# Kernel optimization log

Measured on AMD Instinct MI355X. Metric: run time of the kernel, lower is better.

Reference implementation:

```python
import jax, jax.numpy as jnp
import numpy as np

DETECTIONS_PER_IMG = 36
NMS_THRESH = 0.5
SCORE_THRESH = 0.2
MIN_SIZE = 0.01
NMS_TOPK = 2048  # fixed candidate budget for jit-compatible NMS
BBOX_XFORM_CLIP = float(np.log(1000.0 / 16.0))
WX, WY, WW, WH = 10.0, 10.0, 5.0, 5.0  # torchvision BoxCoder weights


def _decode(reg, props):
    # reg: [N, C*4], props: [N, 4] -> decoded boxes [N, C, 4] (torchvision BoxCoder.decode)
    widths = props[:, 2] - props[:, 0]
    heights = props[:, 3] - props[:, 1]
    ctr_x = props[:, 0] + 0.5 * widths
    ctr_y = props[:, 1] + 0.5 * heights
    reg = reg.reshape(reg.shape[0], -1, 4)
    dx = reg[..., 0] / WX
    dy = reg[..., 1] / WY
    dw = jnp.minimum(reg[..., 2] / WW, BBOX_XFORM_CLIP)
    dh = jnp.minimum(reg[..., 3] / WH, BBOX_XFORM_CLIP)
    pcx = dx * widths[:, None] + ctr_x[:, None]
    pcy = dy * heights[:, None] + ctr_y[:, None]
    pw = jnp.exp(dw) * widths[:, None]
    ph = jnp.exp(dh) * heights[:, None]
    return jnp.stack([pcx - 0.5 * pw, pcy - 0.5 * ph,
                      pcx + 0.5 * pw, pcy + 0.5 * ph], axis=-1)


def _pairwise_iou(boxes):
    # boxes: [K, 4] -> IoU [K, K]
    area = (boxes[:, 2] - boxes[:, 0]) * (boxes[:, 3] - boxes[:, 1])
    lt = jnp.maximum(boxes[:, None, :2], boxes[None, :, :2])
    rb = jnp.minimum(boxes[:, None, 2:], boxes[None, :, 2:])
    wh = jnp.clip(rb - lt, 0.0)
    inter = wh[..., 0] * wh[..., 1]
    union = area[:, None] + area[None, :] - inter
    return jnp.where(union > 0, inter / union, 0.0)


def _per_image(logits, reg, props, feats, img_hw):
    # logits [N, C], reg [N, C*4], props [N, 4], feats [N, D], img_hw [2] (h, w)
    N, C = logits.shape
    boxes = _decode(reg, props)[:, 1:, :].reshape(-1, 4)     # drop background, [N*(C-1), 4]
    scores = jax.nn.softmax(logits, axis=-1)[:, 1:].reshape(-1)
    h = img_hw[0].astype(boxes.dtype)
    w = img_hw[1].astype(boxes.dtype)
    x1 = jnp.clip(boxes[:, 0], 0.0, w)
    y1 = jnp.clip(boxes[:, 1], 0.0, h)
    x2 = jnp.clip(boxes[:, 2], 0.0, w)
    y2 = jnp.clip(boxes[:, 3], 0.0, h)
    boxes = jnp.stack([x1, y1, x2, y2], axis=-1)
    # score threshold + remove_small_boxes as a validity mask
    valid = (scores > SCORE_THRESH) & ((x2 - x1) >= MIN_SIZE) & ((y2 - y1) >= MIN_SIZE)
    masked = jnp.where(valid, scores, -jnp.inf)
    top_s, top_i = jax.lax.top_k(masked, NMS_TOPK)          # candidates in score order
    tboxes = boxes[top_i]
    tvalid = jnp.isfinite(top_s)
    iou = _pairwise_iou(tboxes)                              # [K, K]
    ar = jnp.arange(NMS_TOPK)

    def body(i, keep):
        sup = keep[i] & (iou[i] > NMS_THRESH) & (ar > i)
        return keep & ~sup

    keep = jax.lax.fori_loop(0, NMS_TOPK, body, tvalid)
    # first DETECTIONS_PER_IMG kept candidates, in score order (stable sort: kept first)
    order = jnp.argsort(jnp.where(keep, 0, 1), stable=True)[:DETECTIONS_PER_IMG]
    sel_keep = keep[order]
    prop_idx = top_i[order] // (C - 1)                       # candidate -> proposal row
    out = feats[prop_idx] * sel_keep[:, None].astype(feats.dtype)  # zero-pad missing slots
    return out


def setup_inputs() -> dict:
    key = jax.random.key(0)
    k0, k1, k2, k3, k4 = jax.random.split(key, 5)
    B, N, C, D = 8, 1000, 91, 1024
    class_logits = jax.random.normal(k0, (B, N, C), dtype=jnp.float32) * 3.0
    box_regression = jax.random.normal(k1, (B, N, C * 4), dtype=jnp.float32) * 0.5
    xy = jax.random.uniform(k2, (B, N, 2), minval=0.0, maxval=700.0)
    wh = jax.random.uniform(k3, (B, N, 2), minval=20.0, maxval=100.0)
    proposals = jnp.concatenate([xy, xy + wh], axis=-1).astype(jnp.float32)
    box_features = jax.random.normal(k4, (B, N, D), dtype=jnp.float32)
    image_shapes = jnp.full((B, 2), 800, dtype=jnp.int32)
    return {"class_logits": class_logits, "box_regression": box_regression,
            "proposals": proposals, "box_features": box_features,
            "image_shapes": image_shapes}


def reference(class_logits, box_regression, proposals, box_features, image_shapes):
    # returns [B, DETECTIONS_PER_IMG, D]
    return jax.vmap(_per_image)(class_logits, box_regression, proposals,
                                box_features, image_shapes)
```

## Files before the change

kernel.cpp:

```cpp
#include <hip/hip_runtime.h>
#include <stdint.h>

#define B 8
#define N 1000
#define C 91
#define NC 90
#define D 1024
#define KMAX 2048
#define PAD 4096
#define DETS 36
#define SCORE_THRESH 0.2f
#define NMS_THRESH 0.5f
#define MIN_SIZE 0.01f
#define XFORM_CLIP 4.135166556742356f

__device__ __forceinline__ void decode_clip(const float* __restrict__ rg,
                                            float wdt, float hgt, float cx, float cy,
                                            float W, float H,
                                            float& x1, float& y1, float& x2, float& y2) {
    float dx = rg[0] / 10.0f;
    float dy = rg[1] / 10.0f;
    float dw = fminf(rg[2] / 5.0f, XFORM_CLIP);
    float dh = fminf(rg[3] / 5.0f, XFORM_CLIP);
    float pcx = dx * wdt + cx;
    float pcy = dy * hgt + cy;
    float pw  = expf(dw) * wdt;
    float ph  = expf(dh) * hgt;
    x1 = fminf(fmaxf(pcx - 0.5f * pw, 0.0f), W);
    y1 = fminf(fmaxf(pcy - 0.5f * ph, 0.0f), H);
    x2 = fminf(fmaxf(pcx + 0.5f * pw, 0.0f), W);
    y2 = fminf(fmaxf(pcy + 0.5f * ph, 0.0f), H);
}

__global__ __launch_bounds__(256) void k_score(const float* __restrict__ logits,
                        const float* __restrict__ reg,
                        const float* __restrict__ props,
                        const int* __restrict__ img_hw,
                        unsigned long long* __restrict__ keys) {
    int b = blockIdx.x / 250;
    int local = blockIdx.x % 250;
    int wib = threadIdx.x >> 6, lane = threadIdx.x & 63;
    int n = local * 4 + wib;
    int r = b * N + n;

    __shared__ unsigned long long slot[4][4];
    if (threadIdx.x < 16) slot[threadIdx.x >> 2][threadIdx.x & 3] = 0ULL;
    __syncthreads();

    const float* lg = logits + (size_t)r * C;
    float v0 = lg[lane];
    float v1 = (lane < C - 64) ? lg[64 + lane] : -3.4e38f;
    float m = fmaxf(v0, v1);
    #pragma unroll
    for (int off = 32; off; off >>= 1) m = fmaxf(m, __shfl_xor(m, off, 64));
    float e0 = expf(v0 - m);
    float e1 = (lane < C - 64) ? expf(v1 - m) : 0.0f;
    float s = e0 + e1;
    #pragma unroll
    for (int off = 32; off; off >>= 1) s += __shfl_xor(s, off, 64);

    float p0 = props[r * 4 + 0], p1 = props[r * 4 + 1];
    float p2 = props[r * 4 + 2], p3 = props[r * 4 + 3];
    float wdt = p2 - p0, hgt = p3 - p1;
    float cx = p0 + 0.5f * wdt, cy = p1 + 0.5f * hgt;
    float H = (float)img_hw[b * 2 + 0];
    float W = (float)img_hw[b * 2 + 1];

    unsigned long long keyv[2] = {0ULL, 0ULL};
    #pragma unroll
    for (int t2 = 0; t2 < 2; ++t2) {
        int c = lane + t2 * 64;
        float e = t2 ? e1 : e0;
        if (c >= 1 && c < C) {
            float sc = e / s;
            if (sc > SCORE_THRESH) {
                const float* rg = reg + (size_t)r * (C * 4) + (size_t)c * 4;
                float x1, y1, x2, y2;
                decode_clip(rg, wdt, hgt, cx, cy, W, H, x1, y1, x2, y2);
                if ((x2 - x1) >= MIN_SIZE && (y2 - y1) >= MIN_SIZE) {
                    unsigned int idx = (unsigned int)(n * NC + (c - 1));
                    keyv[t2] = ((unsigned long long)__float_as_uint(sc) << 32) |
                               (unsigned long long)(0xFFFFFFFFu - idx);
                }
            }
        }
    }
    unsigned long long m0 = __ballot(keyv[0] != 0ULL);
    unsigned long long m1 = __ballot(keyv[1] != 0ULL);
    unsigned long long lower = (1ULL << lane) - 1ULL;
    if (keyv[0]) slot[wib][__popcll(m0 & lower)] = keyv[0];
    if (keyv[1]) slot[wib][__popcll(m0) + __popcll(m1 & lower)] = keyv[1];
    __syncthreads();
    if (threadIdx.x < 16) {
        int ww = threadIdx.x >> 2, p = threadIdx.x & 3;
        keys[(size_t)b * PAD + (size_t)(local * 4 + ww) * 4 + p] = slot[ww][p];
    }
}

__global__ __launch_bounds__(512) void k_rank(int* __restrict__ Kvals,
                                              const unsigned long long* __restrict__ keys,
                                              const float* __restrict__ reg,
                                              const float* __restrict__ props,
                                              const int* __restrict__ img_hw,
                                              float* __restrict__ bx1, float* __restrict__ by1,
                                              float* __restrict__ bx2, float* __restrict__ by2,
                                              int* __restrict__ propn) {
    __shared__ unsigned long long sk[PAD];
    __shared__ int partial[8][256];
    int b = blockIdx.y;
    const unsigned long long* kb = keys + (size_t)b * PAD;
    for (int t = threadIdx.x; t < PAD; t += 512)
        sk[t] = (t < 4 * N) ? kb[t] : 0ULL;
    __syncthreads();

    int w = threadIdx.x >> 6;
    int lane = threadIdx.x & 63;
    int rbase = blockIdx.x * 256;
    unsigned long long my0 = sk[rbase + lane];
    unsigned long long my1 = sk[rbase + lane + 64];
    unsigned long long my2 = sk[rbase + lane + 128];
    unsigned long long my3 = sk[rbase + lane + 192];
    int c0 = 0, c1 = 0, c2 = 0, c3 = 0;
    int base = w * 512;
    #pragma unroll 8
    for (int it = 0; it < 512; ++it) {
        unsigned long long k = sk[base + it];
        c0 += (k > my0) ? 1 : 0;
        c1 += (k > my1) ? 1 : 0;
        c2 += (k > my2) ? 1 : 0;
        c3 += (k > my3) ? 1 : 0;
    }
    partial[w][lane]       = c0;
    partial[w][lane + 64]  = c1;
    partial[w][lane + 128] = c2;
    partial[w][lane + 192] = c3;
    __syncthreads();

    if (threadIdx.x < 256) {
        int rl = threadIdx.x;
        int rank = 0;
        #pragma unroll
        for (int q = 0; q < 8; ++q) rank += partial[q][rl];
        int row = rbase + rl;
        unsigned long long my = sk[row];
        if (row == 4 * N) Kvals[b] = (rank < KMAX) ? rank : KMAX;
        if (my != 0ULL && rank < KMAX) {
            unsigned int idx = 0xFFFFFFFFu - (unsigned int)(my & 0xFFFFFFFFull);
            int n = (int)(idx / NC);
            int c = (int)(idx % NC) + 1;
            int r = b * N + n;
            float p0 = props[r * 4 + 0], p1 = props[r * 4 + 1];
            float p2 = props[r * 4 + 2], p3 = props[r * 4 + 3];
            float wdt = p2 - p0, hgt = p3 - p1;
            float cx = p0 + 0.5f * wdt, cy = p1 + 0.5f * hgt;
            float H = (float)img_hw[b * 2 + 0];
            float W = (float)img_hw[b * 2 + 1];
            const float* rg = reg + (size_t)r * (C * 4) + (size_t)c * 4;
            float x1, y1, x2, y2;
            decode_clip(rg, wdt, hgt, cx, cy, W, H, x1, y1, x2, y2);
            size_t o = (size_t)b * KMAX + rank;
            bx1[o] = x1; by1[o] = y1; bx2[o] = x2; by2[o] = y2;
            propn[o] = n;
        }
    }
}

__global__ __launch_bounds__(256) void k_nmsg(const int* __restrict__ Kvals,
                                              const float* __restrict__ bx1, const float* __restrict__ by1,
                                              const float* __restrict__ bx2, const float* __restrict__ by2,
                                              const int* __restrict__ propn,
                                              const float* __restrict__ feats,
                                              float* __restrict__ out) {
    __shared__ float kx1[DETS], ky1[DETS], kx2[DETS], ky2[DETS];
    __shared__ int kpn[DETS];
    __shared__ int skept;
    int b = blockIdx.x, lane = threadIdx.x;

    if (threadIdx.x < 64) {
        int K = Kvals[b];
        size_t ofs = (size_t)b * KMAX;
        int kept = 0;
        for (int cs = 0; cs < K && kept < DETS; cs += 64) {
            int j = cs + lane;
            bool inr = (j < K);
            int jj = inr ? j : 0;
            float x1 = bx1[ofs + jj], y1 = by1[ofs + jj];
            float x2 = bx2[ofs + jj], y2 = by2[ofs + jj];
            int pn = propn[ofs + jj];
            float area = (x2 - x1) * (y2 - y1);

            bool supp = !inr;
            for (int k = 0; k < kept; ++k) {
                float c1 = kx1[k], c2 = ky1[k], c3 = kx2[k], c4 = ky2[k];
                float carea = (c3 - c1) * (c4 - c2);
                float ix1 = fmaxf(c1, x1), iy1 = fmaxf(c2, y1);
                float ix2 = fminf(c3, x2), iy2 = fminf(c4, y2);
                float iw = fmaxf(ix2 - ix1, 0.0f), ih = fmaxf(iy2 - iy1, 0.0f);
                float inter = iw * ih;
                float uni = carea + area - inter;
                float iou = (uni > 0.0f) ? (inter / uni) : 0.0f;
                supp = supp || (iou > NMS_THRESH);
            }
            unsigned long long live = __ballot(!supp);
            while (live != 0ULL && kept < DETS) {
                int i = __ffsll((unsigned long long)live) - 1;
                float c1 = __shfl(x1, i, 64), c2 = __shfl(y1, i, 64);
                float c3 = __shfl(x2, i, 64), c4 = __shfl(y2, i, 64);
                int   cp = __shfl(pn, i, 64);
                if (lane == 0) { kx1[kept] = c1; ky1[kept] = c2; kx2[kept] = c3; ky2[kept] = c4; kpn[kept] = cp; }
                kept++;
                float carea = (c3 - c1) * (c4 - c2);
                float ix1 = fmaxf(c1, x1), iy1 = fmaxf(c2, y1);
                float ix2 = fminf(c3, x2), iy2 = fminf(c4, y2);
                float iw = fmaxf(ix2 - ix1, 0.0f), ih = fmaxf(iy2 - iy1, 0.0f);
                float inter = iw * ih;
                float uni = carea + area - inter;
                float iou = (uni > 0.0f) ? (inter / uni) : 0.0f;
                live &= ~__ballot(iou > NMS_THRESH);
            }
        }
        if (lane == 0) skept = kept;
    }
    __syncthreads();

    int kept = skept;
    int t = threadIdx.x;
    const float4* f4 = (const float4*)feats;
    float4* o4 = (float4*)out;
    for (int s = 0; s < DETS; ++s) {
        float4 v = make_float4(0.f, 0.f, 0.f, 0.f);
        if (s < kept) v = f4[((size_t)b * N + kpn[s]) * (D / 4) + t];
        o4[((size_t)b * DETS + s) * (D / 4) + t] = v;
    }
}

extern "C" void kernel_launch(void* const* d_in, const int* in_sizes, int n_in,
                              void* d_out, int out_size, void* d_ws, size_t ws_size,
                              hipStream_t stream) {
    const float* logits = (const float*)d_in[0];
    const float* reg    = (const float*)d_in[1];
    const float* props  = (const float*)d_in[2];
    const float* feats  = (const float*)d_in[3];
    const int*   img    = (const int*)d_in[4];
    float* out = (float*)d_out;

    char* ws = (char*)d_ws;
    int* Kvals    = (int*)(ws + 0);
    unsigned long long* keys = (unsigned long long*)(ws + 4096);
    float* bx1 = (float*)(ws + 270336);
    float* by1 = (float*)(ws + 335872);
    float* bx2 = (float*)(ws + 401408);
    float* by2 = (float*)(ws + 466944);
    int*   propn = (int*)(ws + 532480);

    k_score<<<dim3(B * 250), dim3(256), 0, stream>>>(logits, reg, props, img, keys);
    k_rank<<<dim3(16, B), dim3(512), 0, stream>>>(Kvals, keys,
        reg, props, img, bx1, by1, bx2, by2, propn);
    k_nmsg<<<dim3(B), dim3(256), 0, stream>>>(Kvals, bx1, by1, bx2, by2, propn, feats, out);
}
```

Baseline: 131.4 us.

## Fuse score, rank and NMS kernels into one persistent kernel with grid barriers

Merges the three kernel launches into one 256-block persistent kernel that uses atomic-counter grid barriers between the scoring, ranking and NMS/gather phases, sharing LDS through a union. The intent is to cut launch overhead and inter-kernel gaps. The final feature copy now uses all 512 threads, each half handling alternate detection slots. The change adds a memset launch and spin-wait barriers, which rely on all 256 blocks being co-resident; it also adds a stray IoU line that reads an uninitialized variable, though its value is immediately overwritten.

```diff
diff --git a/kernel.cpp b/kernel.cpp
--- a/kernel.cpp
+++ b/kernel.cpp
@@ -13,6 +13,8 @@
 #define NMS_THRESH 0.5f
 #define MIN_SIZE 0.01f
 #define XFORM_CLIP 4.135166556742356f
+#define NBLK 256
+#define NTHR 512
 
 __device__ __forceinline__ void decode_clip(const float* __restrict__ rg,
                                             float wdt, float hgt, float cx, float cy,
@@ -32,150 +34,149 @@
     y2 = fminf(fmaxf(pcy + 0.5f * ph, 0.0f), H);
 }
 
-__global__ __launch_bounds__(256) void k_score(const float* __restrict__ logits,
-                        const float* __restrict__ reg,
-                        const float* __restrict__ props,
-                        const int* __restrict__ img_hw,
-                        unsigned long long* __restrict__ keys) {
-    int b = blockIdx.x / 250;
-    int local = blockIdx.x % 250;
-    int wib = threadIdx.x >> 6, lane = threadIdx.x & 63;
-    int n = local * 4 + wib;
-    int r = b * N + n;
-
-    __shared__ unsigned long long slot[4][4];
-    if (threadIdx.x < 16) slot[threadIdx.x >> 2][threadIdx.x & 3] = 0ULL;
+__device__ __forceinline__ void gridbar(int* cnt) {
     __syncthreads();
-
-    const float* lg = logits + (size_t)r * C;
-    float v0 = lg[lane];
-    float v1 = (lane < C - 64) ? lg[64 + lane] : -3.4e38f;
-    float m = fmaxf(v0, v1);
-    #pragma unroll
-    for (int off = 32; off; off >>= 1) m = fmaxf(m, __shfl_xor(m, off, 64));
-    float e0 = expf(v0 - m);
-    float e1 = (lane < C - 64) ? expf(v1 - m) : 0.0f;
-    float s = e0 + e1;
-    #pragma unroll
-    for (int off = 32; off; off >>= 1) s += __shfl_xor(s, off, 64);
-
-    float p0 = props[r * 4 + 0], p1 = props[r * 4 + 1];
-    float p2 = props[r * 4 + 2], p3 = props[r * 4 + 3];
-    float wdt = p2 - p0, hgt = p3 - p1;
-    float cx = p0 + 0.5f * wdt, cy = p1 + 0.5f * hgt;
-    float H = (float)img_hw[b * 2 + 0];
-    float W = (float)img_hw[b * 2 + 1];
-
-    unsigned long long keyv[2] = {0ULL, 0ULL};
-    #pragma unroll
-    for (int t2 = 0; t2 < 2; ++t2) {
-        int c = lane + t2 * 64;
-        float e = t2 ? e1 : e0;
-        if (c >= 1 && c < C) {
-            float sc = e / s;
-            if (sc > SCORE_THRESH) {
-                const float* rg = reg + (size_t)r * (C * 4) + (size_t)c * 4;
-                float x1, y1, x2, y2;
-                decode_clip(rg, wdt, hgt, cx, cy, W, H, x1, y1, x2, y2);
-                if ((x2 - x1) >= MIN_SIZE && (y2 - y1) >= MIN_SIZE) {
-                    unsigned int idx = (unsigned int)(n * NC + (c - 1));
-                    keyv[t2] = ((unsigned long long)__float_as_uint(sc) << 32) |
-                               (unsigned long long)(0xFFFFFFFFu - idx);
-                }
-            }
-        }
-    }
-    unsigned long long m0 = __ballot(keyv[0] != 0ULL);
-    unsigned long long m1 = __ballot(keyv[1] != 0ULL);
-    unsigned long long lower = (1ULL << lane) - 1ULL;
-    if (keyv[0]) slot[wib][__popcll(m0 & lower)] = keyv[0];
-    if (keyv[1]) slot[wib][__popcll(m0) + __popcll(m1 & lower)] = keyv[1];
+    if (threadIdx.x == 0) {
+        __threadfence();
+        atomicAdd(cnt, 1);
+        while (atomicAdd(cnt, 0) < NBLK)
+            __builtin_amdgcn_s_sleep(2);
+        __threadfence();
+    }
     __syncthreads();
-    if (threadIdx.x < 16) {
-        int ww = threadIdx.x >> 2, p = threadIdx.x & 3;
-        keys[(size_t)b * PAD + (size_t)(local * 4 + ww) * 4 + p] = slot[ww][p];
-    }
-}
-
-__global__ __launch_bounds__(512) void k_rank(int* __restrict__ Kvals,
-                                              const unsigned long long* __restrict__ keys,
-                                              const float* __restrict__ reg,
-                                              const float* __restrict__ props,
-                                              const int* __restrict__ img_hw,
-                                              float* __restrict__ bx1, float* __restrict__ by1,
-                                              float* __restrict__ bx2, float* __restrict__ by2,
-                                              int* __restrict__ propn) {
-    __shared__ unsigned long long sk[PAD];
-    __shared__ int partial[8][256];
-    int b = blockIdx.y;
-    const unsigned long long* kb = keys + (size_t)b * PAD;
-    for (int t = threadIdx.x; t < PAD; t += 512)
-        sk[t] = (t < 4 * N) ? kb[t] : 0ULL;
-    __syncthreads();
-
-    int w = threadIdx.x >> 6;
-    int lane = threadIdx.x & 63;
-    int rbase = blockIdx.x * 256;
-    unsigned long long my0 = sk[rbase + lane];
-    unsigned long long my1 = sk[rbase + lane + 64];
-    unsigned long long my2 = sk[rbase + lane + 128];
-    unsigned long long my3 = sk[rbase + lane + 192];
-    int c0 = 0, c1 = 0, c2 = 0, c3 = 0;
-    int base = w * 512;
-    #pragma unroll 8
-    for (int it = 0; it < 512; ++it) {
-        unsigned long long k = sk[base + it];
-        c0 += (k > my0) ? 1 : 0;
-        c1 += (k > my1) ? 1 : 0;
-        c2 += (k > my2) ? 1 : 0;
-        c3 += (k > my3) ? 1 : 0;
-    }
-    partial[w][lane]       = c0;
-    partial[w][lane + 64]  = c1;
-    partial[w][lane + 128] = c2;
-    partial[w][lane + 192] = c3;
-    __syncthreads();
-
-    if (threadIdx.x < 256) {
-        int rl = threadIdx.x;
-        int rank = 0;
-        #pragma unroll
-        for (int q = 0; q < 8; ++q) rank += partial[q][rl];
-        int row = rbase + rl;
-        unsigned long long my = sk[row];
-        if (row == 4 * N) Kvals[b] = (rank < KMAX) ? rank : KMAX;
-        if (my != 0ULL && rank < KMAX) {
-            unsigned int idx = 0xFFFFFFFFu - (unsigned int)(my & 0xFFFFFFFFull);
-            int n = (int)(idx / NC);
-            int c = (int)(idx % NC) + 1;
-            int r = b * N + n;
+}
+
+__global__ __launch_bounds__(NTHR) void k_fused(
+        const float* __restrict__ logits, const float* __restrict__ reg,
+        const float* __restrict__ props,  const int* __restrict__ img_hw,
+        const float* __restrict__ feats,  float* __restrict__ out,
+        int* __restrict__ bar, unsigned long long* __restrict__ keys,
+        int* __restrict__ Kvals,
+        float* __restrict__ bx1, float* __restrict__ by1,
+        float* __restrict__ bx2, float* __restrict__ by2,
+        int* __restrict__ propn) {
+
+    __shared__ union {
+        unsigned long long slot[8][4];
+        struct { unsigned long long sk[PAD]; int partial[8][128]; } p2;
+        struct { float kx1[DETS], ky1[DETS], kx2[DETS], ky2[DETS];
+                 int kpn[DETS]; int skept; } p3;
+    } sm;
+
+    int g = blockIdx.x;
+    int w = threadIdx.x >> 6, lane = threadIdx.x & 63;
+
+    for (int i = 0; i < 4; ++i) {
+        int r = (g * 8 + w) * 4 + i;
+        if (r < B * N) {
+            int b = r / N, n = r % N;
+            if (lane < 4) sm.slot[w][lane] = 0ULL;
+
+            const float* lg = logits + (size_t)r * C;
+            float v0 = lg[lane];
+            float v1 = (lane < C - 64) ? lg[64 + lane] : -3.4e38f;
+            float m = fmaxf(v0, v1);
+            #pragma unroll
+            for (int off = 32; off; off >>= 1) m = fmaxf(m, __shfl_xor(m, off, 64));
+            float e0 = expf(v0 - m);
+            float e1 = (lane < C - 64) ? expf(v1 - m) : 0.0f;
+            float s = e0 + e1;
+            #pragma unroll
+            for (int off = 32; off; off >>= 1) s += __shfl_xor(s, off, 64);
+
             float p0 = props[r * 4 + 0], p1 = props[r * 4 + 1];
             float p2 = props[r * 4 + 2], p3 = props[r * 4 + 3];
             float wdt = p2 - p0, hgt = p3 - p1;
             float cx = p0 + 0.5f * wdt, cy = p1 + 0.5f * hgt;
             float H = (float)img_hw[b * 2 + 0];
             float W = (float)img_hw[b * 2 + 1];
-            const float* rg = reg + (size_t)r * (C * 4) + (size_t)c * 4;
-            float x1, y1, x2, y2;
-            decode_clip(rg, wdt, hgt, cx, cy, W, H, x1, y1, x2, y2);
-            size_t o = (size_t)b * KMAX + rank;
-            bx1[o] = x1; by1[o] = y1; bx2[o] = x2; by2[o] = y2;
-            propn[o] = n;
-        }
-    }
-}
-
-__global__ __launch_bounds__(256) void k_nmsg(const int* __restrict__ Kvals,
-                                              const float* __restrict__ bx1, const float* __restrict__ by1,
-                                              const float* __restrict__ bx2, const float* __restrict__ by2,
-                                              const int* __restrict__ propn,
-                                              const float* __restrict__ feats,
-                                              float* __restrict__ out) {
-    __shared__ float kx1[DETS], ky1[DETS], kx2[DETS], ky2[DETS];
-    __shared__ int kpn[DETS];
-    __shared__ int skept;
-    int b = blockIdx.x, lane = threadIdx.x;
-
+
+            unsigned long long keyv[2] = {0ULL, 0ULL};
+            #pragma unroll
+            for (int t2 = 0; t2 < 2; ++t2) {
+                int c = lane + t2 * 64;
+                float e = t2 ? e1 : e0;
+                if (c >= 1 && c < C) {
+                    float sc = e / s;
+                    if (sc > SCORE_THRESH) {
+                        const float* rg = reg + (size_t)r * (C * 4) + (size_t)c * 4;
+                        float x1, y1, x2, y2;
+                        decode_clip(rg, wdt, hgt, cx, cy, W, H, x1, y1, x2, y2);
+                        if ((x2 - x1) >= MIN_SIZE && (y2 - y1) >= MIN_SIZE) {
+                            unsigned int idx = (unsigned int)(n * NC + (c - 1));
+                            keyv[t2] = ((unsigned long long)__float_as_uint(sc) << 32) |
+                                       (unsigned long long)(0xFFFFFFFFu - idx);
+                        }
+                    }
+                }
+            }
+            unsigned long long m0 = __ballot(keyv[0] != 0ULL);
+            unsigned long long m1 = __ballot(keyv[1] != 0ULL);
+            unsigned long long lower = (1ULL << lane) - 1ULL;
+            if (keyv[0]) sm.slot[w][__popcll(m0 & lower)] = keyv[0];
+            if (keyv[1]) sm.slot[w][__popcll(m0) + __popcll(m1 & lower)] = keyv[1];
+            if (lane < 4)
+                keys[(size_t)b * PAD + (size_t)n * 4 + lane] = sm.slot[w][lane];
+        }
+    }
+
+    gridbar(&bar[0]);
+
+    {
+        int b = g >> 5, sub = g & 31;
+        const unsigned long long* kb = keys + (size_t)b * PAD;
+        for (int t = threadIdx.x; t < PAD; t += NTHR)
+            sm.p2.sk[t] = (t < 4 * N) ? kb[t] : 0ULL;
+        __syncthreads();
+
+        int rbase = sub * 128;
+        unsigned long long my0 = sm.p2.sk[rbase + lane];
+        unsigned long long my1 = sm.p2.sk[rbase + lane + 64];
+        int c0 = 0, c1 = 0;
+        int base = w * 512;
+        #pragma unroll 8
+        for (int it = 0; it < 512; ++it) {
+            unsigned long long k = sm.p2.sk[base + it];
+            c0 += (k > my0) ? 1 : 0;
+            c1 += (k > my1) ? 1 : 0;
+        }
+        sm.p2.partial[w][lane]      = c0;
+        sm.p2.partial[w][lane + 64] = c1;
+        __syncthreads();
+
+        if (threadIdx.x < 128) {
+            int rl = threadIdx.x;
+            int rank = 0;
+            #pragma unroll
+            for (int q = 0; q < 8; ++q) rank += sm.p2.partial[q][rl];
+            int row = rbase + rl;
+            unsigned long long my = sm.p2.sk[row];
+            if (row == 4 * N) Kvals[b] = (rank < KMAX) ? rank : KMAX;
+            if (my != 0ULL && rank < KMAX) {
+                unsigned int idx = 0xFFFFFFFFu - (unsigned int)(my & 0xFFFFFFFFull);
+                int n = (int)(idx / NC);
+                int c = (int)(idx % NC) + 1;
+                int r = b * N + n;
+                float p0 = props[r * 4 + 0], p1 = props[r * 4 + 1];
+                float p2 = props[r * 4 + 2], p3 = props[r * 4 + 3];
+                float wdt = p2 - p0, hgt = p3 - p1;
+                float cx = p0 + 0.5f * wdt, cy = p1 + 0.5f * hgt;
+                float H = (float)img_hw[b * 2 + 0];
+                float W = (float)img_hw[b * 2 + 1];
+                const float* rg = reg + (size_t)r * (C * 4) + (size_t)c * 4;
+                float x1, y1, x2, y2;
+                decode_clip(rg, wdt, hgt, cx, cy, W, H, x1, y1, x2, y2);
+                size_t o = (size_t)b * KMAX + rank;
+                bx1[o] = x1; by1[o] = y1; bx2[o] = x2; by2[o] = y2;
+                propn[o] = n;
+            }
+        }
+    }
+
+    gridbar(&bar[1]);
+    if (g >= B) return;
+
+    int b = g;
     if (threadIdx.x < 64) {
         int K = Kvals[b];
         size_t ofs = (size_t)b * KMAX;
@@ -191,7 +192,8 @@
 
             bool supp = !inr;
             for (int k = 0; k < kept; ++k) {
-                float c1 = kx1[k], c2 = ky1[k], c3 = kx2[k], c4 = ky2[k];
+                float c1 = sm.p3.kx1[k], c2 = sm.p3.ky1[k];
+                float c3 = sm.p3.kx2[k], c4 = sm.p3.ky2[k];
                 float carea = (c3 - c1) * (c4 - c2);
                 float ix1 = fmaxf(c1, x1), iy1 = fmaxf(c2, y1);
                 float ix2 = fminf(c3, x2), iy2 = fminf(c4, y2);
@@ -207,7 +209,9 @@
                 float c1 = __shfl(x1, i, 64), c2 = __shfl(y1, i, 64);
                 float c3 = __shfl(x2, i, 64), c4 = __shfl(y2, i, 64);
                 int   cp = __shfl(pn, i, 64);
-                if (lane == 0) { kx1[kept] = c1; ky1[kept] = c2; kx2[kept] = c3; ky2[kept] = c4; kpn[kept] = cp; }
+                if (lane == 0) { sm.p3.kx1[kept] = c1; sm.p3.ky1[kept] = c2;
+                                 sm.p3.kx2[kept] = c3; sm.p3.ky2[kept] = c4;
+                                 sm.p3.kpn[kept] = cp; }
                 kept++;
                 float carea = (c3 - c1) * (c4 - c2);
                 float ix1 = fmaxf(c1, x1), iy1 = fmaxf(c2, y1);
@@ -215,21 +219,23 @@
                 float iw = fmaxf(ix2 - ix1, 0.0f), ih = fmaxf(iy2 - iy1, 0.0f);
                 float inter = iw * ih;
                 float uni = carea + area - inter;
-                float iou = (uni > 0.0f) ? (inter / uni) : 0.0f;
+                float iou = (uni > 0.0f) ? (inter / iou == iou ? uni : uni) : 0.0f;
+                iou = (uni > 0.0f) ? (inter / uni) : 0.0f;
                 live &= ~__ballot(iou > NMS_THRESH);
             }
         }
-        if (lane == 0) skept = kept;
+        if (lane == 0) sm.p3.skept = kept;
     }
     __syncthreads();
 
-    int kept = skept;
-    int t = threadIdx.x;
+    int kept = sm.p3.skept;
+    int half = threadIdx.x >> 8;
+    int t = threadIdx.x & 255;
     const float4* f4 = (const float4*)feats;
     float4* o4 = (float4*)out;
-    for (int s = 0; s < DETS; ++s) {
+    for (int s = half; s < DETS; s += 2) {
         float4 v = make_float4(0.f, 0.f, 0.f, 0.f);
-        if (s < kept) v = f4[((size_t)b * N + kpn[s]) * (D / 4) + t];
+        if (s < kept) v = f4[((size_t)b * N + sm.p3.kpn[s]) * (D / 4) + t];
         o4[((size_t)b * DETS + s) * (D / 4) + t] = v;
     }
 }
@@ -245,7 +251,8 @@
     float* out = (float*)d_out;
 
     char* ws = (char*)d_ws;
-    int* Kvals    = (int*)(ws + 0);
+    int* bar     = (int*)(ws + 0);
+    int* Kvals   = (int*)(ws + 128);
     unsigned long long* keys = (unsigned long long*)(ws + 4096);
     float* bx1 = (float*)(ws + 270336);
     float* by1 = (float*)(ws + 335872);
@@ -253,8 +260,8 @@
     float* by2 = (float*)(ws + 466944);
     int*   propn = (int*)(ws + 532480);
 
-    k_score<<<dim3(B * 250), dim3(256), 0, stream>>>(logits, reg, props, img, keys);
-    k_rank<<<dim3(16, B), dim3(512), 0, stream>>>(Kvals, keys,
-        reg, props, img, bx1, by1, bx2, by2, propn);
-    k_nmsg<<<dim3(B), dim3(256), 0, stream>>>(Kvals, bx1, by1, bx2, by2, propn, feats, out);
-}
+    hipMemsetAsync(bar, 0, 64, stream);
+    k_fused<<<dim3(NBLK), dim3(NTHR), 0, stream>>>(
+        logits, reg, props, img, feats, out,
+        bar, keys, Kvals, bx1, by1, bx2, by2, propn);
+}
```

New measurement: 163.7 us. 1.25x slower.
